# Optimization experiments

Measured on AMD Instinct MI355X. Metric: run time of the kernel, lower is better.

The kernel has to match this reference:

```python
import jax, jax.numpy as jnp
import numpy as np

B, T, C, H = 4, 4096, 2048, 128


def setup_inputs() -> dict:
    key = jax.random.key(0)
    ks = jax.random.split(key, 7)
    s = 0.02
    return {
        "x": jax.random.normal(ks[0], (B, T, C), dtype=jnp.float32),
        "Wk": jax.random.normal(ks[1], (C, H), dtype=jnp.float32) * s,
        "bk": jax.random.normal(ks[2], (H,), dtype=jnp.float32) * s,
        "Wq": jax.random.normal(ks[3], (C, H), dtype=jnp.float32) * s,
        "bq": jax.random.normal(ks[4], (H,), dtype=jnp.float32) * s,
        "Wv": jax.random.normal(ks[5], (C, H), dtype=jnp.float32) * s,
        "bv": jax.random.normal(ks[6], (H,), dtype=jnp.float32) * s,
    }


def reference(x, Wk, bk, Wq, bq, Wv, bv):
    # x: [B, T, C]
    Bq, Tq, Cq = x.shape
    k = x @ Wk + bk  # [B, T, H]
    q = x @ Wq + bq
    v = x @ Wv + bv
    # NOTE: original scales by C**-0.5 (input emb dim), faithfully reproduced.
    scale = jnp.asarray(Cq, x.dtype) ** -0.5
    wei = jnp.einsum("bth,bsh->bts", q, k) * scale  # [B, T, T]
    causal = jnp.tril(jnp.ones((Tq, Tq), dtype=bool))
    wei = jnp.where(causal, wei, -jnp.inf)
    wei = jax.nn.softmax(wei, axis=-1)
    # dropout omitted (inference/eval mode)
    return jnp.einsum("bts,bsh->bth", wei, v)  # [B, T, H]
```

## Files before the change

kernel.cpp:

```cpp
#include <hip/hip_runtime.h>
#include <hip/hip_bf16.h>
#include <stdint.h>

#define T_SEQ 4096
#define C_DIM 2048
#define H_DIM 128
#define NBATCH 4

typedef unsigned short u16;
typedef __attribute__((ext_vector_type(8))) __bf16 bf16x8;
typedef __attribute__((ext_vector_type(4))) float f32x4;
typedef __attribute__((ext_vector_type(8))) unsigned short u16x8;
typedef __attribute__((ext_vector_type(4))) unsigned short u16x4;

__device__ __forceinline__ u16 f2bf(float f) {
  union { float f; uint32_t i; } v; v.f = f;
  uint32_t r = v.i + 0x7FFFu + ((v.i >> 16) & 1u);
  return (u16)(r >> 16);
}
__device__ __forceinline__ float bf2f(u16 u) {
  union { uint32_t i; float f; } v; v.i = ((uint32_t)u) << 16;
  return v.f;
}

__device__ __forceinline__ void gload16(const void* g, void* l) {
  __builtin_amdgcn_global_load_lds(
      (__attribute__((address_space(1))) void*)(g),
      (__attribute__((address_space(3))) void*)(l), 16, 0, 0);
}

__device__ __forceinline__ f32x4 mfma_bf16(bf16x8 a, bf16x8 b, f32x4 c) {
  return __builtin_amdgcn_mfma_f32_16x16x32_bf16(a, b, c, 0, 0, 0);
}

template<int CTRL>
__device__ __forceinline__ float dpp_mov(float x) {
  return __int_as_float(__builtin_amdgcn_mov_dpp(__float_as_int(x), CTRL, 0xF, 0xF, true));
}
__device__ __forceinline__ float red16_max(float v) {
  v = fmaxf(v, dpp_mov<0x121>(v));
  v = fmaxf(v, dpp_mov<0x122>(v));
  v = fmaxf(v, dpp_mov<0x124>(v));
  v = fmaxf(v, dpp_mov<0x128>(v));
  return v;
}
__device__ __forceinline__ float red16_sum(float v) {
  v += dpp_mov<0x121>(v);
  v += dpp_mov<0x122>(v);
  v += dpp_mov<0x124>(v);
  v += dpp_mov<0x128>(v);
  return v;
}

__global__ __launch_bounds__(256) void transpose_w(
    const float* __restrict__ Wq, const float* __restrict__ Wk,
    const float* __restrict__ Wv, u16* __restrict__ Wt)
{
  __shared__ u16 Wl[64 * 72];
  const int bk = blockIdx.x;
  const int bn = blockIdx.y;
  const int p  = blockIdx.z;
  const float* W = (p == 0) ? Wq : (p == 1) ? Wk : Wv;
  const int t = threadIdx.x;

  for (int ps = 0; ps < 16; ++ps) {
    int e  = ps * 256 + t;
    int kk = e >> 6, nn = e & 63;
    Wl[kk * 72 + nn] = f2bf(W[(size_t)(bk * 64 + kk) * H_DIM + bn * 64 + nn]);
  }
  __syncthreads();
  for (int ps = 0; ps < 16; ++ps) {
    int o  = ps * 256 + t;
    int nl = o >> 6, kl = o & 63;
    int n  = bn * 64 + nl;
    int g  = kl >> 3, j = kl & 7;
    int ks = ((g ^ (n & 7)) << 3) | j;
    Wt[(size_t)p * (H_DIM * C_DIM) + (size_t)n * C_DIM + bk * 64 + kl] = Wl[ks * 72 + nl];
  }
}

__global__ __launch_bounds__(512, 1) void qkv_fused(
    const float* __restrict__ x, const u16* __restrict__ Wt,
    const float* __restrict__ bq, const float* __restrict__ bk, const float* __restrict__ bv,
    u16* __restrict__ qo, u16* __restrict__ ko, u16* __restrict__ vTo)
{
  __shared__ alignas(16) u16 SMEM[2][28672];

  const int tid  = threadIdx.x;
  const int w    = tid >> 6, lane = tid & 63;
  const int t16  = lane & 15, quad = lane >> 4;
  const int mh   = w >> 2;
  const int nq   = w & 3;
  const int rt   = blockIdx.x;

  f32x4 acc[2][6];
  for (int i = 0; i < 2; ++i)
    for (int j = 0; j < 6; ++j) acc[i][j] = f32x4{0.f, 0.f, 0.f, 0.f};

  const size_t rowBase = (size_t)rt * 64;
  const int arow = tid >> 3;
  const int ag   = tid & 7;
  const float* xrow = &x[(rowBase + arow) * C_DIM + ag * 8];

  float4 a0 = ((const float4*)(xrow))[0];
  float4 a1 = ((const float4*)(xrow))[1];
  {
    u16* As = SMEM[0];
    u16* Bs = SMEM[0] + 4096;
    for (int p = 0; p < 3; ++p) {
      const u16* Wp = Wt + (size_t)p * (H_DIM * C_DIM);
      for (int j = 0; j < 2; ++j) {
        int e8 = (((j << 3) + w) * 64 + lane) * 8;
        int rr = e8 >> 6, kk = e8 & 63;
        gload16(Wp + (size_t)rr * C_DIM + kk, &Bs[p * 8192 + e8]);
      }
    }
    u16x8 pk;
    pk[0] = f2bf(a0.x); pk[1] = f2bf(a0.y); pk[2] = f2bf(a0.z); pk[3] = f2bf(a0.w);
    pk[4] = f2bf(a1.x); pk[5] = f2bf(a1.y); pk[6] = f2bf(a1.z); pk[7] = f2bf(a1.w);
    *(u16x8*)&As[arow * 64 + ((ag ^ (arow & 7)) << 3)] = pk;
  }
  a0 = ((const float4*)(xrow + 64))[0];
  a1 = ((const float4*)(xrow + 64))[1];

  for (int it = 0; it < 32; ++it) {
    const int cur = it & 1, nxt = cur ^ 1;
    __syncthreads();

    if (it + 1 < 32) {
      const int k1 = (it + 1) * 64;
      u16* As = SMEM[nxt];
      u16* Bs = SMEM[nxt] + 4096;
      for (int p = 0; p < 3; ++p) {
        const u16* Wp = Wt + (size_t)p * (H_DIM * C_DIM);
        for (int j = 0; j < 2; ++j) {
          int e8 = (((j << 3) + w) * 64 + lane) * 8;
          int rr = e8 >> 6, kk = e8 & 63;
          gload16(Wp + (size_t)rr * C_DIM + k1 + kk, &Bs[p * 8192 + e8]);
        }
      }
      u16x8 pk;
      pk[0] = f2bf(a0.x); pk[1] = f2bf(a0.y); pk[2] = f2bf(a0.z); pk[3] = f2bf(a0.w);
      pk[4] = f2bf(a1.x); pk[5] = f2bf(a1.y); pk[6] = f2bf(a1.z); pk[7] = f2bf(a1.w);
      *(u16x8*)&As[arow * 64 + ((ag ^ (arow & 7)) << 3)] = pk;
      if (it + 2 < 32) {
        const float4* xp = (const float4*)(xrow + (it + 2) * 64);
        a0 = xp[0]; a1 = xp[1];
      }
    }

    u16* As = SMEM[cur];
    u16* Bs = SMEM[cur] + 4096;
    for (int ks = 0; ks < 2; ++ks) {
      bf16x8 af[2], bfr[6];
      for (int ra = 0; ra < 2; ++ra)
        af[ra] = *(const bf16x8*)&As[(mh * 32 + ra * 16 + t16) * 64 +
                                     (((ks * 4 + quad) ^ (t16 & 7)) << 3)];
      for (int c = 0; c < 6; ++c) {
        int col = nq * 96 + c * 16 + t16;
        int p = col >> 7, pc = col & 127;
        bfr[c] = *(const bf16x8*)&Bs[p * 8192 + pc * 64 +
                                     (((ks * 4 + quad) ^ (t16 & 7)) << 3)];
      }
      for (int ra = 0; ra < 2; ++ra)
        for (int c = 0; c < 6; ++c)
          acc[ra][c] = mfma_bf16(af[ra], bfr[c], acc[ra][c]);
    }
  }

  __syncthreads();
  u16* Oq = SMEM[0];
  u16* Ok = SMEM[0] + 8192;
  u16* Ov = SMEM[0] + 16384;

  for (int c = 0; c < 6; ++c) {
    int col = nq * 96 + c * 16 + t16;
    int p = col >> 7, pc = col & 127;
    float bias = (p == 0) ? bq[pc] : (p == 1) ? bk[pc] : bv[pc];
    for (int ra = 0; ra < 2; ++ra) {
      for (int r = 0; r < 4; ++r) {
        int row16 = mh * 32 + ra * 16 + quad * 4 + r;
        float v = acc[ra][c][r] + bias;
        if (p == 2) {
          int gt = row16 >> 3;
          Ov[pc * 64 + ((gt ^ (pc & 7)) << 3) + (row16 & 7)] = f2bf(v);
        } else {
          u16* O = (p == 0) ? Oq : Ok;
          int g = pc >> 3;
          O[row16 * 128 + (((g ^ (row16 & 15)) << 3) | (pc & 7))] = f2bf(v);
        }
      }
    }
  }
  __syncthreads();

  const int bb = rt >> 6;
  const int tb = (rt & 63) * 64;
  for (int ps = 0; ps < 2; ++ps) {
    int c = ps * 512 + tid;
    {
      int row16 = c >> 4, g = c & 15;
      u16x8 v = *(const u16x8*)&Oq[row16 * 128 + ((g ^ (row16 & 15)) << 3)];
      *(u16x8*)&qo[(rowBase + row16) * H_DIM + g * 8] = v;
    }
    *(u16x8*)&ko[rowBase * H_DIM + c * 8] = *(const u16x8*)&Ok[c * 8];
    {
      int d = c >> 3, gc = c & 7;
      *(u16x8*)&vTo[((size_t)bb * H_DIM + d) * T_SEQ + tb + gc * 8] =
          *(const u16x8*)&Ov[c * 8];
    }
  }
}

__global__ __launch_bounds__(256, 2) void flash_attn(
    const u16* __restrict__ q, const u16* __restrict__ k,
    const u16* __restrict__ vT, float* __restrict__ out,
    void* __restrict__ OpartRaw, float* __restrict__ MLpart,
    int split, int pf32)
{
  __shared__ alignas(16) u16 Kt[2][64 * 128];
  __shared__ alignas(16) u16 Vt[2][128 * 64];
  __shared__ alignas(16) u16 Ps[4][32 * 64];

  const int tid  = threadIdx.x;
  const int w    = tid >> 6, lane = tid & 63;
  const int t16  = lane & 15, quad = lane >> 4;
  const int b    = blockIdx.x;

  int qt, kt0, ktn, mls, esd;
  if (split) {
    const int j = blockIdx.y;
    int cidx, n;
    if (j < 32)      { qt = 31 - (j >> 2); cidx = j & 3; n = 4; }
    else if (j < 56) { int t = j - 32; int d3 = t / 3; qt = 23 - d3; cidx = t - d3 * 3; n = 3; }
    else if (j < 72) { int t = j - 56; qt = 15 - (t >> 1); cidx = t & 1; n = 2; }
    else             { qt = 79 - j; cidx = 0; n = 1; }
    const int NT = 2 * qt + 2;
    kt0 = cidx * NT / n;
    ktn = (cidx + 1) * NT / n - kt0;
    if (n == 1) { mls = -1; esd = -1; }
    else {
      int mlb, esb;
      if (qt >= 24)      { mlb = (qt - 24) * 4;      esb = (qt - 24) * 3; }
      else if (qt >= 16) { mlb = 32 + (qt - 16) * 3; esb = 24 + (qt - 16) * 2; }
      else               { mlb = 56 + (qt - 8) * 2;  esb = 40 + (qt - 8); }
      mls = b * 72 + mlb + cidx;
      esd = (cidx >= 1) ? (b * 48 + esb + cidx - 1) : -2;
    }
  } else {
    qt = 31 - blockIdx.y; kt0 = 0; ktn = 2 * qt + 2; mls = -1; esd = -1;
  }

  const float SCALE = 0.022097086912079612f;
  const float L2E   = 1.4426950408889634f;

  bf16x8 qf[2][4];
  for (int rh = 0; rh < 2; ++rh) {
    const u16* qrow = q + ((size_t)(b * T_SEQ + qt * 128 + w * 32 + rh * 16 + t16)) * H_DIM;
    for (int c = 0; c < 4; ++c)
      qf[rh][c] = *(const bf16x8*)(qrow + c * 32 + quad * 8);
  }

  f32x4 Oc[2][8];
  for (int rh = 0; rh < 2; ++rh)
    for (int i = 0; i < 8; ++i) Oc[rh][i] = f32x4{0.f, 0.f, 0.f, 0.f};
  float mrow[2][4], lrow[2][4];
  for (int rh = 0; rh < 2; ++rh)
    for (int r = 0; r < 4; ++r) { mrow[rh][r] = -1e30f; lrow[rh][r] = 0.f; }

  const u16* kbase = k  + ((size_t)b * T_SEQ) * H_DIM;
  const u16* vbase = vT + ((size_t)b * H_DIM) * T_SEQ;

  {
    const u16* kg = kbase + (size_t)(kt0 * 64) * H_DIM;
    for (int j = 0; j < 4; ++j) {
      int e8 = (((j << 2) + w) * 64 + lane) * 8;
      gload16(kg + e8, &Kt[0][e8]);
      int d = e8 >> 6, kk = e8 & 63;
      gload16(vbase + (size_t)d * T_SEQ + kt0 * 64 + kk, &Vt[0][e8]);
    }
  }

  int cur = 0;
  for (int it = 0; it < ktn; ++it) {
    const int kt = kt0 + it;
    __syncthreads();
    if (it + 1 < ktn) {
      const int nb = cur ^ 1, kt1 = kt + 1;
      const u16* kg = kbase + (size_t)(kt1 * 64) * H_DIM;
      for (int j = 0; j < 4; ++j) {
        int e8 = (((j << 2) + w) * 64 + lane) * 8;
        gload16(kg + e8, &Kt[nb][e8]);
        int d = e8 >> 6, kk = e8 & 63;
        gload16(vbase + (size_t)d * T_SEQ + kt1 * 64 + kk, &Vt[nb][e8]);
      }
    }

    f32x4 S[2][4];
    for (int rh = 0; rh < 2; ++rh)
      for (int ct = 0; ct < 4; ++ct) S[rh][ct] = f32x4{0.f, 0.f, 0.f, 0.f};

    __builtin_amdgcn_s_setprio(1);
    for (int c = 0; c < 4; ++c)
      for (int ct = 0; ct < 4; ++ct) {
        bf16x8 kf = *(const bf16x8*)&Kt[cur][(ct * 16 + t16) * H_DIM +
                                            (((c * 4 + quad) ^ t16) << 3)];
        S[0][ct] = mfma_bf16(qf[0][c], kf, S[0][ct]);
        S[1][ct] = mfma_bf16(qf[1][c], kf, S[1][ct]);
      }
    __builtin_amdgcn_s_setprio(0);

    const int kb0 = kt * 64;
    for (int rh = 0; rh < 2; ++rh) {
      const int r0 = qt * 128 + w * 32 + rh * 16;
      const bool needmask = (kb0 + 63 > r0);
      for (int ct = 0; ct < 4; ++ct)
        for (int r = 0; r < 4; ++r) {
          float s = S[rh][ct][r] * SCALE;
          if (needmask && (kb0 + ct * 16 + t16 > r0 + quad * 4 + r)) s = -1e30f;
          S[rh][ct][r] = s;
        }
    }

    float alpha[2][4];
    for (int rh = 0; rh < 2; ++rh)
      for (int r = 0; r < 4; ++r) {
        float mx = red16_max(fmaxf(fmaxf(S[rh][0][r], S[rh][1][r]),
                                   fmaxf(S[rh][2][r], S[rh][3][r])));
        float mn = fmaxf(mrow[rh][r], mx);
        alpha[rh][r] = exp2f((mrow[rh][r] - mn) * L2E);
        mrow[rh][r] = mn;
        float ssum = 0.f;
        for (int ct = 0; ct < 4; ++ct) {
          float pv = exp2f((S[rh][ct][r] - mn) * L2E);
          S[rh][ct][r] = pv;
          ssum += pv;
        }
        lrow[rh][r] = lrow[rh][r] * alpha[rh][r] + red16_sum(ssum);
      }
    for (int rh = 0; rh < 2; ++rh)
      for (int dt = 0; dt < 8; ++dt)
        for (int r = 0; r < 4; ++r)
          Oc[rh][dt][r] *= alpha[rh][r];

    u16* pw = Ps[w];
    for (int rh = 0; rh < 2; ++rh)
      for (int ct = 0; ct < 4; ++ct)
        for (int r = 0; r < 4; ++r) {
          int row = rh * 16 + quad * 4 + r;
          pw[row * 64 + ((((ct << 1) | (t16 >> 3)) ^ (row & 7)) << 3) + (t16 & 7)]
              = f2bf(S[rh][ct][r]);
        }
    __asm__ volatile("s_waitcnt lgkmcnt(0)" ::: "memory");

    __builtin_amdgcn_s_setprio(1);
    for (int ks = 0; ks < 2; ++ks) {
      bf16x8 pf0 = *(const bf16x8*)&pw[t16 * 64 + (((ks * 4 + quad) ^ (t16 & 7)) << 3)];
      bf16x8 pf1 = *(const bf16x8*)&pw[(16 + t16) * 64 + (((ks * 4 + quad) ^ (t16 & 7)) << 3)];
      for (int dt = 0; dt < 8; ++dt) {
        bf16x8 vf = *(const bf16x8*)&Vt[cur][(dt * 16 + t16) * 64 +
                                            (((ks * 4 + quad) ^ (t16 & 7)) << 3)];
        Oc[0][dt] = mfma_bf16(pf0, vf, Oc[0][dt]);
        Oc[1][dt] = mfma_bf16(pf1, vf, Oc[1][dt]);
      }
    }
    __builtin_amdgcn_s_setprio(0);
    cur ^= 1;
  }

  if (mls < 0) {
    for (int rh = 0; rh < 2; ++rh)
      for (int r = 0; r < 4; ++r) {
        float inv = 1.0f / lrow[rh][r];
        size_t row = (size_t)b * T_SEQ + qt * 128 + w * 32 + rh * 16 + quad * 4 + r;
        for (int dt = 0; dt < 8; ++dt)
          out[row * H_DIM + dt * 16 + t16] = Oc[rh][dt][r] * inv;
      }
  } else {
    if (t16 == 0)
      for (int rh = 0; rh < 2; ++rh)
        for (int r = 0; r < 4; ++r) {
          int row = w * 32 + rh * 16 + quad * 4 + r;
          MLpart[(size_t)mls * 256 + row * 2 + 0] = mrow[rh][r];
          MLpart[(size_t)mls * 256 + row * 2 + 1] = lrow[rh][r];
        }
    if (esd == -2) {
      for (int rh = 0; rh < 2; ++rh)
        for (int r = 0; r < 4; ++r) {
          size_t row = (size_t)b * T_SEQ + qt * 128 + w * 32 + rh * 16 + quad * 4 + r;
          for (int dt = 0; dt < 8; ++dt)
            out[row * H_DIM + dt * 16 + t16] = Oc[rh][dt][r];
        }
    } else if (pf32) {
      float* op = (float*)OpartRaw + (size_t)esd * 16384;
      for (int rh = 0; rh < 2; ++rh)
        for (int r = 0; r < 4; ++r) {
          int row = w * 32 + rh * 16 + quad * 4 + r;
          for (int dt = 0; dt < 8; ++dt)
            op[row * 128 + dt * 16 + t16] = Oc[rh][dt][r];
        }
    } else {
      u16* op = (u16*)OpartRaw + (size_t)esd * 16384;
      for (int rh = 0; rh < 2; ++rh)
        for (int r = 0; r < 4; ++r) {
          int row = w * 32 + rh * 16 + quad * 4 + r;
          for (int dt = 0; dt < 8; ++dt)
            op[row * 128 + dt * 16 + t16] = f2bf(Oc[rh][dt][r]);
        }
    }
  }
}

__global__ __launch_bounds__(256) void combine(
    const void* __restrict__ OpartRaw, const float* __restrict__ MLpart,
    float* __restrict__ out, int pf32)
{
  __shared__ float cs[4][128];
  const float L2E = 1.4426950408889634f;
  const int s = blockIdx.x;
  const int b = s / 24, qt = 8 + (s % 24);
  const int t = threadIdx.x;

  int n, mlb, esb;
  if (qt >= 24)      { n = 4; mlb = (qt - 24) * 4;      esb = (qt - 24) * 3; }
  else if (qt >= 16) { n = 3; mlb = 32 + (qt - 16) * 3; esb = 24 + (qt - 16) * 2; }
  else               { n = 2; mlb = 56 + (qt - 8) * 2;  esb = 40 + (qt - 8); }
  const int mls0 = b * 72 + mlb;
  const int esd0 = b * 48 + esb;

  if (t < 128) {
    float m[4], l[4];
    float mg = -1e30f;
    for (int c = 0; c < n; ++c) {
      const float* ML = MLpart + (size_t)(mls0 + c) * 256;
      m[c] = ML[t * 2]; l[c] = ML[t * 2 + 1];
      mg = fmaxf(mg, m[c]);
    }
    float denom = 0.f, e[4];
    for (int c = 0; c < n; ++c) {
      e[c] = exp2f((m[c] - mg) * L2E);
      denom += l[c] * e[c];
    }
    float inv = 1.0f / denom;
    for (int c = 0; c < n; ++c) cs[c][t] = e[c] * inv;
  }
  __syncthreads();

  float* o = out + ((size_t)b * T_SEQ + (size_t)qt * 128) * (size_t)H_DIM;
  for (int i4 = t; i4 < 4096; i4 += 256) {
    const int row = i4 >> 5;
    float4 acc = ((float4*)o)[i4];
    const float c0 = cs[0][row];
    acc.x *= c0; acc.y *= c0; acc.z *= c0; acc.w *= c0;
    for (int c = 1; c < n; ++c) {
      const float cc = cs[c][row];
      if (pf32) {
        const float4 p = ((const float4*)((const float*)OpartRaw +
                          (size_t)(esd0 + c - 1) * 16384))[i4];
        acc.x += p.x * cc; acc.y += p.y * cc;
        acc.z += p.z * cc; acc.w += p.w * cc;
      } else {
        const u16x4 p = ((const u16x4*)((const u16*)OpartRaw +
                         (size_t)(esd0 + c - 1) * 16384))[i4];
        acc.x += bf2f(p[0]) * cc; acc.y += bf2f(p[1]) * cc;
        acc.z += bf2f(p[2]) * cc; acc.w += bf2f(p[3]) * cc;
      }
    }
    ((float4*)o)[i4] = acc;
  }
}

extern "C" void kernel_launch(void* const* d_in, const int* in_sizes, int n_in,
                              void* d_out, int out_size, void* d_ws, size_t ws_size,
                              hipStream_t stream) {
  const float* x  = (const float*)d_in[0];
  const float* Wk = (const float*)d_in[1];
  const float* bk = (const float*)d_in[2];
  const float* Wq = (const float*)d_in[3];
  const float* bq = (const float*)d_in[4];
  const float* Wv = (const float*)d_in[5];
  const float* bv = (const float*)d_in[6];
  float* out = (float*)d_out;

  char* ws = (char*)d_ws;
  u16* qb  = (u16*)(ws);
  u16* kb  = (u16*)(ws + 4194304);
  u16* vT  = (u16*)(ws + 8388608);
  u16* Wt  = (u16*)(ws + 12582912);
  void* Opart = (void*)(ws + 14155776);

  const size_t base     = 14155776ull;
  const size_t ml_bytes = 294912ull;
  const size_t need_f32 = base + 12582912ull + ml_bytes;
  const size_t need_b16 = base + 6291456ull  + ml_bytes;

  int split, pf32;
  float* MLpart;
  if (ws_size >= need_f32) {
    split = 1; pf32 = 1;
    MLpart = (float*)(ws + base + 12582912ull);
  } else if (ws_size >= need_b16) {
    split = 1; pf32 = 0;
    MLpart = (float*)(ws + base + 6291456ull);
  } else {
    split = 0; pf32 = 0;
    MLpart = (float*)(ws + base);
  }

  hipLaunchKernelGGL(transpose_w, dim3(32, 2, 3), dim3(256), 0, stream, Wq, Wk, Wv, Wt);
  hipLaunchKernelGGL(qkv_fused, dim3(256), dim3(512), 0, stream,
                     x, Wt, bq, bk, bv, qb, kb, vT);
  hipLaunchKernelGGL(flash_attn, dim3(4, split ? 80 : 32), dim3(256), 0, stream,
                     qb, kb, vT, out, Opart, MLpart, split, pf32);
  if (split)
    hipLaunchKernelGGL(combine, dim3(96), dim3(256), 0, stream, Opart, MLpart, out, pf32);
}
```

Baseline: 311.8 us.

## Halve flash-attention query tile to 64 rows and double split-KV grid

Reduces each flash_attn block's query tile from 128 to 64 rows (16 per wave), doubling the number of query tiles and blocks (160 per batch with split-KV, 64 without). The split schedule, partial-result indexing, and the combine kernel are remapped to the new tile count. The P staging buffer is changed from an XOR-swizzled layout to a padded 72-wide stride. This aims to improve occupancy and load balance across CUs, but each K/V tile is now reused by half as many query rows, which doubles K/V global and LDS traffic per unit of work.

```diff
diff --git a/kernel.cpp b/kernel.cpp
--- a/kernel.cpp
+++ b/kernel.cpp
@@ -220,7 +220,7 @@
 {
   __shared__ alignas(16) u16 Kt[2][64 * 128];
   __shared__ alignas(16) u16 Vt[2][128 * 64];
-  __shared__ alignas(16) u16 Ps[4][32 * 64];
+  __shared__ alignas(16) u16 Ps[4 * 16 * 72];
 
   const int tid  = threadIdx.x;
   const int w    = tid >> 6, lane = tid & 63;
@@ -230,43 +230,41 @@
   int qt, kt0, ktn, mls, esd;
   if (split) {
     const int j = blockIdx.y;
-    int cidx, n;
-    if (j < 32)      { qt = 31 - (j >> 2); cidx = j & 3; n = 4; }
-    else if (j < 56) { int t = j - 32; int d3 = t / 3; qt = 23 - d3; cidx = t - d3 * 3; n = 3; }
-    else if (j < 72) { int t = j - 56; qt = 15 - (t >> 1); cidx = t & 1; n = 2; }
-    else             { qt = 79 - j; cidx = 0; n = 1; }
-    const int NT = 2 * qt + 2;
-    kt0 = cidx * NT / n;
-    ktn = (cidx + 1) * NT / n - kt0;
+    int c, n;
+    if (j < 64)       { qt = 63 - (j >> 2); c = j & 3; n = 4; }
+    else if (j < 112) { int t = j - 64; int d3 = t / 3; qt = 47 - d3; c = t - d3 * 3; n = 3; }
+    else if (j < 144) { int t = j - 112; qt = 31 - (t >> 1); c = t & 1; n = 2; }
+    else              { qt = 159 - j; c = 0; n = 1; }
+    const int NT = qt + 1;
+    kt0 = c * NT / n;
+    ktn = (c + 1) * NT / n - kt0;
     if (n == 1) { mls = -1; esd = -1; }
     else {
       int mlb, esb;
-      if (qt >= 24)      { mlb = (qt - 24) * 4;      esb = (qt - 24) * 3; }
-      else if (qt >= 16) { mlb = 32 + (qt - 16) * 3; esb = 24 + (qt - 16) * 2; }
-      else               { mlb = 56 + (qt - 8) * 2;  esb = 40 + (qt - 8); }
-      mls = b * 72 + mlb + cidx;
-      esd = (cidx >= 1) ? (b * 48 + esb + cidx - 1) : -2;
+      if (qt >= 48)      { mlb = (qt - 48) * 4;       esb = (qt - 48) * 3; }
+      else if (qt >= 32) { mlb = 64 + (qt - 32) * 3;  esb = 48 + (qt - 32) * 2; }
+      else               { mlb = 112 + (qt - 16) * 2; esb = 80 + (qt - 16); }
+      mls = b * 144 + mlb + c;
+      esd = (c >= 1) ? (b * 96 + esb + c - 1) : -2;
     }
   } else {
-    qt = 31 - blockIdx.y; kt0 = 0; ktn = 2 * qt + 2; mls = -1; esd = -1;
+    qt = 63 - blockIdx.y; kt0 = 0; ktn = qt + 1; mls = -1; esd = -1;
   }
 
   const float SCALE = 0.022097086912079612f;
   const float L2E   = 1.4426950408889634f;
 
-  bf16x8 qf[2][4];
-  for (int rh = 0; rh < 2; ++rh) {
-    const u16* qrow = q + ((size_t)(b * T_SEQ + qt * 128 + w * 32 + rh * 16 + t16)) * H_DIM;
+  bf16x8 qf[4];
+  {
+    const u16* qrow = q + ((size_t)(b * T_SEQ + qt * 64 + w * 16 + t16)) * H_DIM;
     for (int c = 0; c < 4; ++c)
-      qf[rh][c] = *(const bf16x8*)(qrow + c * 32 + quad * 8);
-  }
-
-  f32x4 Oc[2][8];
-  for (int rh = 0; rh < 2; ++rh)
-    for (int i = 0; i < 8; ++i) Oc[rh][i] = f32x4{0.f, 0.f, 0.f, 0.f};
-  float mrow[2][4], lrow[2][4];
-  for (int rh = 0; rh < 2; ++rh)
-    for (int r = 0; r < 4; ++r) { mrow[rh][r] = -1e30f; lrow[rh][r] = 0.f; }
+      qf[c] = *(const bf16x8*)(qrow + c * 32 + quad * 8);
+  }
+
+  f32x4 Oc[8];
+  for (int i = 0; i < 8; ++i) Oc[i] = f32x4{0.f, 0.f, 0.f, 0.f};
+  float mrow[4] = {-1e30f, -1e30f, -1e30f, -1e30f};
+  float lrow[4] = {0.f, 0.f, 0.f, 0.f};
 
   const u16* kbase = k  + ((size_t)b * T_SEQ) * H_DIM;
   const u16* vbase = vT + ((size_t)b * H_DIM) * T_SEQ;
@@ -296,72 +294,59 @@
       }
     }
 
-    f32x4 S[2][4];
-    for (int rh = 0; rh < 2; ++rh)
-      for (int ct = 0; ct < 4; ++ct) S[rh][ct] = f32x4{0.f, 0.f, 0.f, 0.f};
-
+    f32x4 S[4];
+    for (int ct = 0; ct < 4; ++ct) S[ct] = f32x4{0.f, 0.f, 0.f, 0.f};
     __builtin_amdgcn_s_setprio(1);
-    for (int c = 0; c < 4; ++c)
+    for (int c = 0; c < 4; ++c) {
       for (int ct = 0; ct < 4; ++ct) {
         bf16x8 kf = *(const bf16x8*)&Kt[cur][(ct * 16 + t16) * H_DIM +
                                             (((c * 4 + quad) ^ t16) << 3)];
-        S[0][ct] = mfma_bf16(qf[0][c], kf, S[0][ct]);
-        S[1][ct] = mfma_bf16(qf[1][c], kf, S[1][ct]);
-      }
+        S[ct] = mfma_bf16(qf[c], kf, S[ct]);
+      }
+    }
     __builtin_amdgcn_s_setprio(0);
 
-    const int kb0 = kt * 64;
-    for (int rh = 0; rh < 2; ++rh) {
-      const int r0 = qt * 128 + w * 32 + rh * 16;
-      const bool needmask = (kb0 + 63 > r0);
-      for (int ct = 0; ct < 4; ++ct)
-        for (int r = 0; r < 4; ++r) {
-          float s = S[rh][ct][r] * SCALE;
-          if (needmask && (kb0 + ct * 16 + t16 > r0 + quad * 4 + r)) s = -1e30f;
-          S[rh][ct][r] = s;
-        }
-    }
-
-    float alpha[2][4];
-    for (int rh = 0; rh < 2; ++rh)
-      for (int r = 0; r < 4; ++r) {
-        float mx = red16_max(fmaxf(fmaxf(S[rh][0][r], S[rh][1][r]),
-                                   fmaxf(S[rh][2][r], S[rh][3][r])));
-        float mn = fmaxf(mrow[rh][r], mx);
-        alpha[rh][r] = exp2f((mrow[rh][r] - mn) * L2E);
-        mrow[rh][r] = mn;
-        float ssum = 0.f;
-        for (int ct = 0; ct < 4; ++ct) {
-          float pv = exp2f((S[rh][ct][r] - mn) * L2E);
-          S[rh][ct][r] = pv;
-          ssum += pv;
-        }
-        lrow[rh][r] = lrow[rh][r] * alpha[rh][r] + red16_sum(ssum);
-      }
-    for (int rh = 0; rh < 2; ++rh)
-      for (int dt = 0; dt < 8; ++dt)
-        for (int r = 0; r < 4; ++r)
-          Oc[rh][dt][r] *= alpha[rh][r];
-
-    u16* pw = Ps[w];
-    for (int rh = 0; rh < 2; ++rh)
-      for (int ct = 0; ct < 4; ++ct)
-        for (int r = 0; r < 4; ++r) {
-          int row = rh * 16 + quad * 4 + r;
-          pw[row * 64 + ((((ct << 1) | (t16 >> 3)) ^ (row & 7)) << 3) + (t16 & 7)]
-              = f2bf(S[rh][ct][r]);
-        }
+    const bool diag = (kt == qt);
+    for (int ct = 0; ct < 4; ++ct)
+      for (int r = 0; r < 4; ++r) {
+        float s = S[ct][r] * SCALE;
+        if (diag && (ct * 16 + t16 > w * 16 + quad * 4 + r)) s = -1e30f;
+        S[ct][r] = s;
+      }
+
+    float alpha[4], mnew[4];
+    for (int r = 0; r < 4; ++r) {
+      float mx = red16_max(fmaxf(fmaxf(S[0][r], S[1][r]), fmaxf(S[2][r], S[3][r])));
+      mnew[r]  = fmaxf(mrow[r], mx);
+      alpha[r] = exp2f((mrow[r] - mnew[r]) * L2E);
+      mrow[r]  = mnew[r];
+    }
+    for (int r = 0; r < 4; ++r) {
+      float s = 0.f;
+      for (int ct = 0; ct < 4; ++ct) {
+        float pv = exp2f((S[ct][r] - mnew[r]) * L2E);
+        S[ct][r] = pv;
+        s += pv;
+      }
+      lrow[r] = lrow[r] * alpha[r] + red16_sum(s);
+    }
+    for (int dt = 0; dt < 8; ++dt)
+      for (int r = 0; r < 4; ++r)
+        Oc[dt][r] *= alpha[r];
+
+    u16* pw = &Ps[w * 1152];
+    for (int ct = 0; ct < 4; ++ct)
+      for (int r = 0; r < 4; ++r)
+        pw[(quad * 4 + r) * 72 + ct * 16 + t16] = f2bf(S[ct][r]);
     __asm__ volatile("s_waitcnt lgkmcnt(0)" ::: "memory");
 
     __builtin_amdgcn_s_setprio(1);
     for (int ks = 0; ks < 2; ++ks) {
-      bf16x8 pf0 = *(const bf16x8*)&pw[t16 * 64 + (((ks * 4 + quad) ^ (t16 & 7)) << 3)];
-      bf16x8 pf1 = *(const bf16x8*)&pw[(16 + t16) * 64 + (((ks * 4 + quad) ^ (t16 & 7)) << 3)];
+      bf16x8 pf = *(const bf16x8*)&pw[t16 * 72 + ks * 32 + quad * 8];
       for (int dt = 0; dt < 8; ++dt) {
         bf16x8 vf = *(const bf16x8*)&Vt[cur][(dt * 16 + t16) * 64 +
                                             (((ks * 4 + quad) ^ (t16 & 7)) << 3)];
-        Oc[0][dt] = mfma_bf16(pf0, vf, Oc[0][dt]);
-        Oc[1][dt] = mfma_bf16(pf1, vf, Oc[1][dt]);
+        Oc[dt] = mfma_bf16(pf, vf, Oc[dt]);
       }
     }
     __builtin_amdgcn_s_setprio(0);
@@ -369,44 +354,39 @@
   }
 
   if (mls < 0) {
-    for (int rh = 0; rh < 2; ++rh)
-      for (int r = 0; r < 4; ++r) {
-        float inv = 1.0f / lrow[rh][r];
-        size_t row = (size_t)b * T_SEQ + qt * 128 + w * 32 + rh * 16 + quad * 4 + r;
-        for (int dt = 0; dt < 8; ++dt)
-          out[row * H_DIM + dt * 16 + t16] = Oc[rh][dt][r] * inv;
-      }
+    for (int r = 0; r < 4; ++r) {
+      float inv = 1.0f / lrow[r];
+      size_t row = (size_t)b * T_SEQ + qt * 64 + w * 16 + quad * 4 + r;
+      for (int dt = 0; dt < 8; ++dt)
+        out[row * H_DIM + dt * 16 + t16] = Oc[dt][r] * inv;
+    }
   } else {
     if (t16 == 0)
-      for (int rh = 0; rh < 2; ++rh)
-        for (int r = 0; r < 4; ++r) {
-          int row = w * 32 + rh * 16 + quad * 4 + r;
-          MLpart[(size_t)mls * 256 + row * 2 + 0] = mrow[rh][r];
-          MLpart[(size_t)mls * 256 + row * 2 + 1] = lrow[rh][r];
-        }
+      for (int r = 0; r < 4; ++r) {
+        int row = w * 16 + quad * 4 + r;
+        MLpart[(size_t)mls * 128 + row * 2 + 0] = mrow[r];
+        MLpart[(size_t)mls * 128 + row * 2 + 1] = lrow[r];
+      }
     if (esd == -2) {
-      for (int rh = 0; rh < 2; ++rh)
-        for (int r = 0; r < 4; ++r) {
-          size_t row = (size_t)b * T_SEQ + qt * 128 + w * 32 + rh * 16 + quad * 4 + r;
-          for (int dt = 0; dt < 8; ++dt)
-            out[row * H_DIM + dt * 16 + t16] = Oc[rh][dt][r];
-        }
+      for (int r = 0; r < 4; ++r) {
+        size_t row = (size_t)b * T_SEQ + qt * 64 + w * 16 + quad * 4 + r;
+        for (int dt = 0; dt < 8; ++dt)
+          out[row * H_DIM + dt * 16 + t16] = Oc[dt][r];
+      }
     } else if (pf32) {
-      float* op = (float*)OpartRaw + (size_t)esd * 16384;
-      for (int rh = 0; rh < 2; ++rh)
-        for (int r = 0; r < 4; ++r) {
-          int row = w * 32 + rh * 16 + quad * 4 + r;
-          for (int dt = 0; dt < 8; ++dt)
-            op[row * 128 + dt * 16 + t16] = Oc[rh][dt][r];
-        }
+      float* op = (float*)OpartRaw + (size_t)esd * 8192;
+      for (int r = 0; r < 4; ++r) {
+        int row = w * 16 + quad * 4 + r;
+        for (int dt = 0; dt < 8; ++dt)
+          op[row * 128 + dt * 16 + t16] = Oc[dt][r];
+      }
     } else {
-      u16* op = (u16*)OpartRaw + (size_t)esd * 16384;
-      for (int rh = 0; rh < 2; ++rh)
-        for (int r = 0; r < 4; ++r) {
-          int row = w * 32 + rh * 16 + quad * 4 + r;
-          for (int dt = 0; dt < 8; ++dt)
-            op[row * 128 + dt * 16 + t16] = f2bf(Oc[rh][dt][r]);
-        }
+      u16* op = (u16*)OpartRaw + (size_t)esd * 8192;
+      for (int r = 0; r < 4; ++r) {
+        int row = w * 16 + quad * 4 + r;
+        for (int dt = 0; dt < 8; ++dt)
+          op[row * 128 + dt * 16 + t16] = f2bf(Oc[dt][r]);
+      }
     }
   }
 }
@@ -415,24 +395,24 @@
     const void* __restrict__ OpartRaw, const float* __restrict__ MLpart,
     float* __restrict__ out, int pf32)
 {
-  __shared__ float cs[4][128];
+  __shared__ float cs[4][64];
   const float L2E = 1.4426950408889634f;
   const int s = blockIdx.x;
-  const int b = s / 24, qt = 8 + (s % 24);
+  const int b = s / 48, qt = 16 + (s % 48);
   const int t = threadIdx.x;
 
   int n, mlb, esb;
-  if (qt >= 24)      { n = 4; mlb = (qt - 24) * 4;      esb = (qt - 24) * 3; }
-  else if (qt >= 16) { n = 3; mlb = 32 + (qt - 16) * 3; esb = 24 + (qt - 16) * 2; }
-  else               { n = 2; mlb = 56 + (qt - 8) * 2;  esb = 40 + (qt - 8); }
-  const int mls0 = b * 72 + mlb;
-  const int esd0 = b * 48 + esb;
-
-  if (t < 128) {
+  if (qt >= 48)      { n = 4; mlb = (qt - 48) * 4;       esb = (qt - 48) * 3; }
+  else if (qt >= 32) { n = 3; mlb = 64 + (qt - 32) * 3;  esb = 48 + (qt - 32) * 2; }
+  else               { n = 2; mlb = 112 + (qt - 16) * 2; esb = 80 + (qt - 16); }
+  const int mls0 = b * 144 + mlb;
+  const int esd0 = b * 96 + esb;
+
+  if (t < 64) {
     float m[4], l[4];
     float mg = -1e30f;
     for (int c = 0; c < n; ++c) {
-      const float* ML = MLpart + (size_t)(mls0 + c) * 256;
+      const float* ML = MLpart + (size_t)(mls0 + c) * 128;
       m[c] = ML[t * 2]; l[c] = ML[t * 2 + 1];
       mg = fmaxf(mg, m[c]);
     }
@@ -446,8 +426,8 @@
   }
   __syncthreads();
 
-  float* o = out + ((size_t)b * T_SEQ + (size_t)qt * 128) * (size_t)H_DIM;
-  for (int i4 = t; i4 < 4096; i4 += 256) {
+  float* o = out + ((size_t)b * T_SEQ + (size_t)qt * 64) * (size_t)H_DIM;
+  for (int i4 = t; i4 < 2048; i4 += 256) {
     const int row = i4 >> 5;
     float4 acc = ((float4*)o)[i4];
     const float c0 = cs[0][row];
@@ -456,12 +436,12 @@
       const float cc = cs[c][row];
       if (pf32) {
         const float4 p = ((const float4*)((const float*)OpartRaw +
-                          (size_t)(esd0 + c - 1) * 16384))[i4];
+                          (size_t)(esd0 + c - 1) * 8192))[i4];
         acc.x += p.x * cc; acc.y += p.y * cc;
         acc.z += p.z * cc; acc.w += p.w * cc;
       } else {
         const u16x4 p = ((const u16x4*)((const u16*)OpartRaw +
-                         (size_t)(esd0 + c - 1) * 16384))[i4];
+                         (size_t)(esd0 + c - 1) * 8192))[i4];
         acc.x += bf2f(p[0]) * cc; acc.y += bf2f(p[1]) * cc;
         acc.z += bf2f(p[2]) * cc; acc.w += bf2f(p[3]) * cc;
       }
@@ -510,8 +490,8 @@
   hipLaunchKernelGGL(transpose_w, dim3(32, 2, 3), dim3(256), 0, stream, Wq, Wk, Wv, Wt);
   hipLaunchKernelGGL(qkv_fused, dim3(256), dim3(512), 0, stream,
                      x, Wt, bq, bk, bv, qb, kb, vT);
-  hipLaunchKernelGGL(flash_attn, dim3(4, split ? 80 : 32), dim3(256), 0, stream,
+  hipLaunchKernelGGL(flash_attn, dim3(4, split ? 160 : 64), dim3(256), 0, stream,
                      qb, kb, vT, out, Opart, MLpart, split, pf32);
   if (split)
-    hipLaunchKernelGGL(combine, dim3(96), dim3(256), 0, stream, Opart, MLpart, out, pf32);
-}
+    hipLaunchKernelGGL(combine, dim3(192), dim3(256), 0, stream, Opart, MLpart, out, pf32);
+}
```

After: 299.1 us. 4.1% less time.
